# Kernel tuning notes

Measured on AMD Instinct MI355X. Metric: run time of the kernel, lower is better.

Reference implementation:

```python
import jax, jax.numpy as jnp
import numpy as np

B, P, K = 32, 1024, 20  # clouds, points per cloud, kNN neighbors
EPS = 1e-5


def knn_idx(x, k):
    # x: [B,P,d] -> indices of k nearest neighbors (squared L2, includes self), [B,P,k]
    d2 = jnp.sum(x * x, axis=-1)
    dist = d2[:, :, None] + d2[:, None, :] - 2.0 * jnp.einsum('bpd,bqd->bpq', x, x)
    _, idx = jax.lax.top_k(-dist, k)
    return idx


def edge_conv(x, idx, msg_fn):
    # gather neighbor features, build [x_i, x_j - x_i] edge features, max-aggregate
    xj = jax.vmap(lambda xb, ib: xb[ib])(x, idx)            # [B,P,K,d]
    xi = jnp.broadcast_to(x[:, :, None, :], xj.shape)       # [B,P,K,d]
    e = jnp.concatenate([xi, xj - xi], axis=-1)             # [B,P,K,2d]
    return jnp.max(msg_fn(e), axis=2)                       # [B,P,out]


def setup_inputs() -> dict:
    key = jax.random.key(0)
    ks = jax.random.split(key, 5)
    s = 0.05
    return {
        'pos': jax.random.normal(ks[0], (B * P, 3), jnp.float32),
        'W1a': jax.random.normal(ks[1], (6, 64), jnp.float32) * s,
        'b1a': jnp.zeros((64,), jnp.float32),
        'g1': jnp.ones((64,), jnp.float32),
        'be1': jnp.zeros((64,), jnp.float32),
        'W1b': jax.random.normal(ks[2], (64, 64), jnp.float32) * s,
        'b1b': jnp.zeros((64,), jnp.float32),
        'W2': jax.random.normal(ks[3], (128, 128), jnp.float32) * s,
        'b2': jnp.zeros((128,), jnp.float32),
        'Wl': jax.random.normal(ks[4], (192, 128), jnp.float32) * s,
        'bl': jnp.zeros((128,), jnp.float32),
        'batch': jnp.repeat(jnp.arange(B, dtype=jnp.int32), P),
    }


def reference(pos, W1a, b1a, g1, be1, W1b, b1b, W2, b2, Wl, bl, batch):
    # batch is uniform-sized and sorted -> fixed reshape to [B,P,.]
    x0 = pos.reshape(B, P, 3)

    def mlp1(e):  # Linear(6,64) -> BatchNorm -> ReLU -> Linear(64,64)
        h = e @ W1a + b1a
        mu = jnp.mean(h, axis=(0, 1, 2))
        var = jnp.var(h, axis=(0, 1, 2))
        h = (h - mu) * jax.lax.rsqrt(var + EPS) * g1 + be1
        h = jax.nn.relu(h)
        return h @ W1b + b1b

    x1 = edge_conv(x0, knn_idx(x0, K), mlp1)                         # [B,P,64]
    x2 = edge_conv(x1, knn_idx(x1, K), lambda e: e @ W2 + b2)        # [B,P,128]
    h = jnp.concatenate([x1, x2], axis=-1) @ Wl + bl                 # [B,P,128]
    return jnp.max(h, axis=1)                                        # global_max_pool -> [B,128]
```

## Files before the change

kernel.cpp:

```cpp
#include <hip/hip_runtime.h>
#include <cfloat>
#include <cstdint>

#define NB 32
#define NP 1024
#define NK 20
#define NPTS 32768

typedef __attribute__((ext_vector_type(8))) short bf16x8;
typedef __attribute__((ext_vector_type(4))) float f32x4;

__device__ __forceinline__ unsigned bf16rne(float v) {
  const unsigned u = __float_as_uint(v);
  return (u + 0x7fffu + ((u >> 16) & 1u)) >> 16;
}

__device__ __forceinline__ float unsort_f(unsigned s) {
  const unsigned m = (~(unsigned)((int)s >> 31)) | 0x80000000u;
  return __uint_as_float(s ^ m);
}

__global__ __launch_bounds__(256) void kd2(const float* __restrict__ x, int dim,
                                           float* __restrict__ d2) {
  int p = blockIdx.x * 256 + threadIdx.x;
  if (p >= NPTS) return;
  if (dim == 64) {
    const float4* xr = (const float4*)(x + (size_t)p * 64);
    float s = 0.f;
#pragma unroll
    for (int dq = 0; dq < 16; dq++) {
      float4 v = xr[dq];
      s = fmaf(v.x, v.x, s);
      s = fmaf(v.y, v.y, s);
      s = fmaf(v.z, v.z, s);
      s = fmaf(v.w, v.w, s);
    }
    d2[p] = s;
  } else {
    float s = 0.f;
#pragma unroll
    for (int d = 0; d < 3; d++) {
      float v = x[p * 3 + d];
      s = fmaf(v, v, s);
    }
    d2[p] = s;
  }
}

__global__ __launch_bounds__(256) void kxprep(const float* __restrict__ x,
                                              unsigned short* __restrict__ Xh,
                                              unsigned short* __restrict__ Xl) {
  const int t = blockIdx.x * 256 + threadIdx.x;
  const int p = t >> 3, g = t & 7;
  const float4* xr = (const float4*)(x + (size_t)p * 64 + g * 8);
  const float4 v0 = xr[0];
  const float4 v1 = xr[1];
  const float vv[8] = {v0.x, v0.y, v0.z, v0.w, v1.x, v1.y, v1.z, v1.w};
  unsigned short h[8], l[8];
#pragma unroll
  for (int j = 0; j < 8; j++) {
    const float z = vv[j];
    const unsigned u = __float_as_uint(z);
    const unsigned hb = (u + 0x7fffu + ((u >> 16) & 1u)) & 0xffff0000u;
    h[j] = (unsigned short)(hb >> 16);
    l[j] = (unsigned short)bf16rne(z - __uint_as_float(hb));
  }
  const int off = (((p >> 4) * 2 + (g >> 2)) * 64 + ((g & 3) << 4) + (p & 15)) * 8;
  *(uint4*)&Xh[off] = *(const uint4*)&h[0];
  *(uint4*)&Xl[off] = *(const uint4*)&l[0];
}

__device__ __forceinline__ void select20(const float* dv, unsigned long long* w,
                                         int lane, int pg, int gbase,
                                         int* __restrict__ idxo) {
  unsigned k32[16];
#pragma unroll
  for (int ii = 0; ii < 16; ii++) {
    unsigned u = __float_as_uint(dv[ii]);
    u ^= (((int)u >> 31) | 0x80000000u);
    k32[ii] = u;
  }
  unsigned lmn = k32[0];
#pragma unroll
  for (int ii = 1; ii < 16; ii++) lmn = k32[ii] < lmn ? k32[ii] : lmn;
  unsigned mn = lmn, mlm = lmn;
#pragma unroll
  for (int s = 1; s < 64; s <<= 1) {
    const unsigned a = __shfl_xor(mn, s, 64);
    const unsigned b = __shfl_xor(mlm, s, 64);
    mn = a < mn ? a : mn;
    mlm = b > mlm ? b : mlm;
  }
  unsigned lo32 = mn;
  unsigned long long hi32 = (unsigned long long)mlm + 1;
  float flo = unsort_f(mn), fhi = unsort_f(mlm);
  float clo = 0.f, chi = 140.f;
  unsigned m32 = 0;
  bool found = false;
  for (int it = 0; it < 40; ++it) {
    if (hi32 - (unsigned long long)lo32 <= 1) break;
    unsigned m;
    if (it < 6) {
      float fr = (42.f - clo) / (chi - clo);
      fr = fr < 0.04f ? 0.04f : (fr > 0.96f ? 0.96f : fr);
      const float pf = fmaf(fhi - flo, fr, flo);
      unsigned u = __float_as_uint(pf);
      u ^= (((int)u >> 31) | 0x80000000u);
      m = u;
      if (m <= lo32) m = lo32 + 1;
      if ((unsigned long long)m >= hi32) m = (unsigned)(hi32 - 1);
    } else {
      m = (unsigned)(lo32 + ((hi32 - lo32) >> 1));
    }
    int cnt = 0;
#pragma unroll
    for (int ii = 0; ii < 16; ii++) cnt += __popcll(__ballot(k32[ii] < m));
    if (cnt < 20) {
      lo32 = m;
      flo = unsort_f(m);
      clo = (float)cnt;
    } else if (cnt > 64) {
      hi32 = m;
      fhi = unsort_f(m);
      chi = (float)cnt;
    } else {
      m32 = m;
      found = true;
      break;
    }
  }

  if (found) {
    unsigned mask = 0;
#pragma unroll
    for (int ii = 0; ii < 16; ii++) mask |= (k32[ii] < m32) ? (1u << ii) : 0u;
    const int lc = __popc(mask);
    int x = lc;
#pragma unroll
    for (int s = 1; s < 64; s <<= 1) {
      const int y = __shfl_up(x, s, 64);
      if (lane >= s) x += y;
    }
    int off = x - lc;
    w[lane] = ~0ULL;
    __builtin_amdgcn_wave_barrier();
#pragma unroll
    for (int i = 0; i < 4; i++)
#pragma unroll
      for (int j = 0; j < 4; j++) {
        const int ii = i * 4 + j;
        if ((mask & (1u << ii)) && off < 64) {
          w[off] = ((unsigned long long)k32[ii] << 10) |
                   (unsigned)(i * 256 + (lane << 2) + j);
          off++;
        }
      }
    __builtin_amdgcn_wave_barrier();
    const unsigned long long K = w[lane];
    int rank = 0;
#pragma unroll
    for (int m = 0; m < 64; m++) rank += (K > w[m]) ? 1 : 0;
    if (K != ~0ULL && rank < NK)
      idxo[(size_t)pg * NK + rank] = gbase + (int)(K & 1023u);
  } else {
    unsigned long long lo64 = ((unsigned long long)lo32) << 10;
    unsigned long long hi64 = hi32 << 10;
    unsigned long long cut = hi64;
    for (int it = 0; it < 48 && (hi64 - lo64) > 1; ++it) {
      const unsigned long long m = lo64 + ((hi64 - lo64) >> 1);
      int cnt = 0;
#pragma unroll
      for (int ii = 0; ii < 16; ii++) {
        const unsigned long long key =
            ((unsigned long long)k32[ii] << 10) |
            (unsigned)(((ii >> 2) << 8) + (lane << 2) + (ii & 3));
        cnt += __popcll(__ballot(key < m));
      }
      if (cnt == 20) {
        cut = m;
        break;
      }
      if (cnt < 20)
        lo64 = m;
      else
        hi64 = m;
      cut = hi64;
    }
    int base = 0;
#pragma unroll
    for (int ii = 0; ii < 16; ii++) {
      const unsigned long long key =
          ((unsigned long long)k32[ii] << 10) |
          (unsigned)(((ii >> 2) << 8) + (lane << 2) + (ii & 3));
      const unsigned long long b = __ballot(key < cut);
      if (key < cut) {
        const int slot = base + __builtin_amdgcn_mbcnt_hi(
                                    (unsigned)(b >> 32),
                                    __builtin_amdgcn_mbcnt_lo((unsigned)b, 0));
        idxo[(size_t)pg * NK + slot] = gbase + (int)(key & 1023u);
      }
      base += __popcll(b);
    }
  }
}

__global__ __launch_bounds__(512) void kfsel1(const float* __restrict__ pos,
                                              const float* __restrict__ d2,
                                              int* __restrict__ idxo) {
  __shared__ float px[1024], py[1024], pz[1024], pd2[1024];
  __shared__ unsigned long long lw[8][64];
  const int tid = threadIdx.x;
  const int lane = tid & 63;
  const int w = tid >> 6;
  const int cloud = blockIdx.x >> 7;
  const int mb = blockIdx.x & 127;
  const int cb = cloud << 10;

  if (tid < 256) {
    const float4* ppos = (const float4*)(pos + (size_t)cb * 3 + tid * 12);
    const float4 a = ppos[0], b = ppos[1], c = ppos[2];
    *(float4*)&px[tid * 4] = make_float4(a.x, a.w, b.z, c.y);
    *(float4*)&py[tid * 4] = make_float4(a.y, b.x, b.w, c.z);
    *(float4*)&pz[tid * 4] = make_float4(a.z, b.y, c.x, c.w);
  }
  *(float2*)&pd2[tid * 2] = *(const float2*)(d2 + cb + tid * 2);
  __syncthreads();

  const int pl = mb * 8 + w;
  const float xi0 = px[pl], xi1 = py[pl], xi2 = pz[pl];
  const float dp = pd2[pl];
  float dv[16];
#pragma unroll
  for (int i = 0; i < 4; i++) {
    const float4 X = *(const float4*)&px[i * 256 + lane * 4];
    const float4 Y = *(const float4*)&py[i * 256 + lane * 4];
    const float4 Z = *(const float4*)&pz[i * 256 + lane * 4];
    const float4 Q = *(const float4*)&pd2[i * 256 + lane * 4];
    const float xs[4] = {X.x, X.y, X.z, X.w};
    const float ys[4] = {Y.x, Y.y, Y.z, Y.w};
    const float zs[4] = {Z.x, Z.y, Z.z, Z.w};
    const float qs[4] = {Q.x, Q.y, Q.z, Q.w};
#pragma unroll
    for (int j = 0; j < 4; j++) {
      float acc = 0.f;
      acc = fmaf(xi0, xs[j], acc);
      acc = fmaf(xi1, ys[j], acc);
      acc = fmaf(xi2, zs[j], acc);
      dv[i * 4 + j] = fmaf(-2.f, acc, dp + qs[j]);
    }
  }
  select20(dv, lw[w], lane, cb + pl, cb, idxo);
}

__global__ __launch_bounds__(512) void kdsel2(const unsigned short* __restrict__ Xh,
                                              const unsigned short* __restrict__ Xl,
                                              const float* __restrict__ d2,
                                              int* __restrict__ idxo) {
  __shared__ __align__(16) float Dl[16][1024];
  __shared__ unsigned long long lw[8][64];
  const int lane = threadIdx.x & 63;
  const int w = threadIdx.x >> 6;
  const int cloud = blockIdx.x & 31;
  const int rb = blockIdx.x >> 5;
  const int cb = cloud * 1024;
  const int rowb = rb * 16;

  bf16x8 Ah[2], Al[2];
#pragma unroll
  for (int ks = 0; ks < 2; ks++) {
    const int tg = (cb + rowb) >> 4;
    const size_t base = ((size_t)(tg * 2 + ks) * 64 + lane) * 8;
    Ah[ks] = *(const bf16x8*)&Xh[base];
    Al[ks] = *(const bf16x8*)&Xl[base];
  }
  float d2r[4];
#pragma unroll
  for (int r = 0; r < 4; r++) d2r[r] = d2[cb + rowb + (lane >> 4) * 4 + r];

#pragma unroll 2
  for (int nt = 0; nt < 8; nt++) {
    const int c0 = w * 128 + nt * 16;
    const int cg = cb + c0;
    bf16x8 Bh2[2], Bl2[2];
#pragma unroll
    for (int ks = 0; ks < 2; ks++) {
      const int tg = cg >> 4;
      const size_t base = ((size_t)(tg * 2 + ks) * 64 + lane) * 8;
      Bh2[ks] = *(const bf16x8*)&Xh[base];
      Bl2[ks] = *(const bf16x8*)&Xl[base];
    }
    const float d2c = d2[cg + (lane & 15)];
    f32x4 C = {0.f, 0.f, 0.f, 0.f};
    C = __builtin_amdgcn_mfma_f32_16x16x32_bf16(Ah[0], Bh2[0], C, 0, 0, 0);
    C = __builtin_amdgcn_mfma_f32_16x16x32_bf16(Ah[0], Bl2[0], C, 0, 0, 0);
    C = __builtin_amdgcn_mfma_f32_16x16x32_bf16(Al[0], Bh2[0], C, 0, 0, 0);
    C = __builtin_amdgcn_mfma_f32_16x16x32_bf16(Ah[1], Bh2[1], C, 0, 0, 0);
    C = __builtin_amdgcn_mfma_f32_16x16x32_bf16(Ah[1], Bl2[1], C, 0, 0, 0);
    C = __builtin_amdgcn_mfma_f32_16x16x32_bf16(Al[1], Bh2[1], C, 0, 0, 0);
#pragma unroll
    for (int r = 0; r < 4; r++) {
      const int row = (lane >> 4) * 4 + r;
      const int col = c0 + (lane & 15);
      Dl[row][col ^ ((row & 7) << 2)] = fmaf(-2.f, C[r], d2r[r] + d2c);
    }
  }
  __syncthreads();

  for (int pp = 0; pp < 2; pp++) {
    const int pl = w * 2 + pp;
    const int s = (pl & 7) << 2;
    float dv[16];
#pragma unroll
    for (int i = 0; i < 4; i++) {
      const float4 d4 = *(const float4*)&Dl[pl][(i * 256 + lane * 4) ^ s];
      dv[i * 4 + 0] = d4.x;
      dv[i * 4 + 1] = d4.y;
      dv[i * 4 + 2] = d4.z;
      dv[i * 4 + 3] = d4.w;
    }
    select20(dv, lw[w], lane, cb + rowb + pl, cb, idxo);
  }
}

__global__ __launch_bounds__(256) void kstats(const float* __restrict__ pos,
                                              const int* __restrict__ idx,
                                              double* __restrict__ Spart) {
  __shared__ float red[4][42];
  const int tid = threadIdx.x;
  const int w = tid >> 6;
  int p = blockIdx.x * 256 + tid;
  float xi0 = pos[p * 3], xi1 = pos[p * 3 + 1], xi2 = pos[p * 3 + 2];
  float s1[6];
  float s2[36];
#pragma unroll
  for (int a = 0; a < 6; a++) s1[a] = 0.f;
#pragma unroll
  for (int a = 0; a < 36; a++) s2[a] = 0.f;
  for (int k = 0; k < NK; k++) {
    int j = idx[p * NK + k];
    float e[6];
    e[0] = xi0;
    e[1] = xi1;
    e[2] = xi2;
    e[3] = pos[j * 3] - xi0;
    e[4] = pos[j * 3 + 1] - xi1;
    e[5] = pos[j * 3 + 2] - xi2;
#pragma unroll
    for (int a = 0; a < 6; a++) {
      s1[a] += e[a];
#pragma unroll
      for (int b = 0; b < 6; b++) s2[a * 6 + b] = fmaf(e[a], e[b], s2[a * 6 + b]);
    }
  }
#pragma unroll
  for (int a = 0; a < 6; a++) {
#pragma unroll
    for (int m = 1; m < 64; m <<= 1) s1[a] += __shfl_xor(s1[a], m, 64);
  }
#pragma unroll
  for (int a = 0; a < 36; a++) {
#pragma unroll
    for (int m = 1; m < 64; m <<= 1) s2[a] += __shfl_xor(s2[a], m, 64);
  }
  if ((tid & 63) == 0) {
#pragma unroll
    for (int a = 0; a < 6; a++) red[w][a] = s1[a];
#pragma unroll
    for (int a = 0; a < 36; a++) red[w][6 + a] = s2[a];
  }
  __syncthreads();
  if (tid < 42) {
    double t = (double)red[0][tid] + (double)red[1][tid] + (double)red[2][tid] +
               (double)red[3][tid];
    Spart[(size_t)blockIdx.x * 42 + tid] = t;
  }
}

__global__ void kbn(const double* __restrict__ Spart, const float* __restrict__ W1a,
                    const float* __restrict__ b1a, const float* __restrict__ g1,
                    const float* __restrict__ be1, const float* __restrict__ W1b,
                    float* __restrict__ ss, unsigned short* __restrict__ Bh,
                    unsigned short* __restrict__ Bl) {
  __shared__ double S[42];
  const int c = threadIdx.x;
  if (c < 42) {
    double t = 0.0;
    for (int b = 0; b < 128; b++) t += Spart[(size_t)b * 42 + c];
    S[c] = t;
  }
  for (int t = c; t < 4096; t += 256) {
    const int j = t & 7, L = (t >> 3) & 63, f = t >> 9;
    const int nt = f >> 1, ks = f & 1;
    const int k = ks * 32 + (L >> 4) * 8 + j;
    const int n = nt * 16 + (L & 15);
    const float wv = W1b[k * 64 + n];
    const unsigned u = __float_as_uint(wv);
    const unsigned hb = (u + 0x7fffu + ((u >> 16) & 1u)) & 0xffff0000u;
    Bh[t] = (unsigned short)(hb >> 16);
    Bl[t] = (unsigned short)bf16rne(wv - __uint_as_float(hb));
  }
  __syncthreads();
  if (c < 64) {
    double w[6];
#pragma unroll
    for (int d = 0; d < 6; d++) w[d] = (double)W1a[d * 64 + c];
    double b = (double)b1a[c];
    const double invN = 1.0 / (double)((size_t)NPTS * NK);
    double m1 = 0.0;
#pragma unroll
    for (int d = 0; d < 6; d++) m1 += w[d] * S[d];
    m1 *= invN;
    double q = 0.0;
#pragma unroll
    for (int a = 0; a < 6; a++)
#pragma unroll
      for (int d = 0; d < 6; d++) q += w[a] * w[d] * S[6 + a * 6 + d];
    q *= invN;
    double mu = m1 + b;
    double eh2 = q + 2.0 * b * m1 + b * b;
    double var = eh2 - mu * mu;
    if (var < 0.0) var = 0.0;
    double inv = 1.0 / sqrt(var + 1e-5);
    double sc = (double)g1[c] * inv;
    ss[c] = (float)sc;
    ss[64 + c] = (float)((double)be1[c] - mu * sc);
  }
}

#define EC1P 8
__global__ __launch_bounds__(256) void kec1(const float* __restrict__ pos,
                                            const int* __restrict__ idx,
                                            const float* __restrict__ ss,
                                            const float* __restrict__ W1a,
                                            const float* __restrict__ b1a,
                                            const unsigned short* __restrict__ Bh,
                                            const unsigned short* __restrict__ Bl,
                                            const float* __restrict__ b1b,
                                            float* __restrict__ x1) {
  __shared__ __align__(16) unsigned short Ah[4][3072];
  __shared__ __align__(16) unsigned short Al[4][3072];
  __shared__ float nbr[4][160];
  const int tid = threadIdx.x;
  const int lane = tid & 63;
  const int w = tid >> 6;
  const int p0 = blockIdx.x * EC1P + w * 2;

  unsigned short* ah = Ah[w];
  unsigned short* al = Al[w];
  float* nb = nbr[w];

  if (lane < 40) {
    const int j = idx[(size_t)p0 * NK + lane];
    nb[lane * 4 + 0] = pos[j * 3 + 0];
    nb[lane * 4 + 1] = pos[j * 3 + 1];
    nb[lane * 4 + 2] = pos[j * 3 + 2];
  }

  float wdf[3], wbt[3];
#pragma unroll
  for (int d = 0; d < 3; d++) {
    const float top = W1a[d * 64 + lane];
    const float bot = W1a[(3 + d) * 64 + lane];
    wdf[d] = top - bot;
    wbt[d] = bot;
  }
  const float b1 = b1a[lane];
  const float sc = ss[lane];
  const float sh = ss[64 + lane];
  const int lanehi = (((lane & 31) >> 3) * 128) + ((lane >> 5) * 512);
  const int lanelo = lane & 7;
  const int g3w = ((lane & 31) >> 3) + ((lane >> 5) << 2);
  __builtin_amdgcn_wave_barrier();

#pragma unroll
  for (int pp = 0; pp < 2; pp++) {
    const int p = p0 + pp;
    const float xi0 = pos[p * 3], xi1 = pos[p * 3 + 1], xi2 = pos[p * 3 + 2];
    const float pu = fmaf(xi2, wdf[2], fmaf(xi1, wdf[1], fmaf(xi0, wdf[0], b1)));
    for (int k = 0; k < NK; k++) {
      const int row = pp * NK + k;
      const float4 nbv = *(const float4*)&nb[row * 4];
      const float pv = fmaf(nbv.z, wbt[2], fmaf(nbv.y, wbt[1], nbv.x * wbt[0]));
      const float z = fmaxf(fmaf(pu + pv, sc, sh), 0.f);
      const unsigned u = __float_as_uint(z);
      const unsigned hb = (u + 0x7fffu + ((u >> 16) & 1u)) & 0xffff0000u;
      const int off =
          (row >> 4) * 1024 + lanehi + (((row & 15) ^ g3w) << 3) + lanelo;
      ah[off] = (unsigned short)(hb >> 16);
      al[off] = (unsigned short)bf16rne(z - __uint_as_float(hb));
    }
  }
  __builtin_amdgcn_wave_barrier();

  bf16x8 bh[4][2], bl[4][2];
#pragma unroll
  for (int nt = 0; nt < 4; nt++)
#pragma unroll
    for (int ks = 0; ks < 2; ks++) {
      const int base = ((nt * 2 + ks) * 64 + lane) * 8;
      bh[nt][ks] = *(const bf16x8*)&Bh[base];
      bl[nt][ks] = *(const bf16x8*)&Bl[base];
    }

  float pA[4], pB[4];
#pragma unroll
  for (int nt = 0; nt < 4; nt++) {
    pA[nt] = -FLT_MAX;
    pB[nt] = -FLT_MAX;
  }
  const int q4 = (lane >> 4) * 4;
  const int rb0 = (lane >> 4) * 128 + (((lane & 15) ^ (lane >> 4)) << 3);
  const int rb1 =
      512 + (lane >> 4) * 128 + (((lane & 15) ^ (4 + (lane >> 4))) << 3);

#pragma unroll
  for (int mt = 0; mt < 3; mt++) {
    const bf16x8 a_h0 = *(const bf16x8*)&ah[mt * 1024 + rb0];
    const bf16x8 a_l0 = *(const bf16x8*)&al[mt * 1024 + rb0];
    const bf16x8 a_h1 = *(const bf16x8*)&ah[mt * 1024 + rb1];
    const bf16x8 a_l1 = *(const bf16x8*)&al[mt * 1024 + rb1];
#pragma unroll
    for (int nt = 0; nt < 4; nt++) {
      f32x4 C = {0.f, 0.f, 0.f, 0.f};
      C = __builtin_amdgcn_mfma_f32_16x16x32_bf16(a_h0, bh[nt][0], C, 0, 0, 0);
      C = __builtin_amdgcn_mfma_f32_16x16x32_bf16(a_h0, bl[nt][0], C, 0, 0, 0);
      C = __builtin_amdgcn_mfma_f32_16x16x32_bf16(a_l0, bh[nt][0], C, 0, 0, 0);
      C = __builtin_amdgcn_mfma_f32_16x16x32_bf16(a_h1, bh[nt][1], C, 0, 0, 0);
      C = __builtin_amdgcn_mfma_f32_16x16x32_bf16(a_h1, bl[nt][1], C, 0, 0, 0);
      C = __builtin_amdgcn_mfma_f32_16x16x32_bf16(a_l1, bh[nt][1], C, 0, 0, 0);
#pragma unroll
      for (int r = 0; r < 4; r++) {
        const int row = mt * 16 + q4 + r;
        const float vv = C[r];
        if (row < NK) pA[nt] = fmaxf(pA[nt], vv);
        if (row >= NK && row < 2 * NK) pB[nt] = fmaxf(pB[nt], vv);
      }
    }
  }
#pragma unroll
  for (int s = 16; s < 64; s <<= 1) {
#pragma unroll
    for (int nt = 0; nt < 4; nt++) {
      pA[nt] = fmaxf(pA[nt], __shfl_xor(pA[nt], s, 64));
      pB[nt] = fmaxf(pB[nt], __shfl_xor(pB[nt], s, 64));
    }
  }
  if (lane < 16) {
#pragma unroll
    for (int nt = 0; nt < 4; nt++) {
      const float bb = b1b[nt * 16 + lane];
      x1[(size_t)p0 * 64 + nt * 16 + lane] = pA[nt] + bb;
      x1[(size_t)(p0 + 1) * 64 + nt * 16 + lane] = pB[nt] + bb;
    }
  }
}

__global__ __launch_bounds__(256) void kv(const float* __restrict__ x1,
                                          const float* __restrict__ W2,
                                          float* __restrict__ v) {
  const int c = threadIdx.x & 127;
  const int sub = threadIdx.x >> 7;
  float wv[64];
#pragma unroll
  for (int d = 0; d < 64; d++) wv[d] = W2[(64 + d) * 128 + c];
  const int pbase = blockIdx.x * 64 + sub * 32;
  for (int i = 0; i < 32; i++) {
    const int p = pbase + i;
    const float4* xr = (const float4*)(x1 + (size_t)p * 64);
    float a0 = 0.f, a1 = 0.f;
#pragma unroll
    for (int dq = 0; dq < 16; dq++) {
      float4 xv = xr[dq];
      a0 = fmaf(xv.x, wv[dq * 4 + 0], a0);
      a1 = fmaf(xv.y, wv[dq * 4 + 1], a1);
      a0 = fmaf(xv.z, wv[dq * 4 + 2], a0);
      a1 = fmaf(xv.w, wv[dq * 4 + 3], a1);
    }
    v[(size_t)p * 128 + c] = a0 + a1;
  }
}

__global__ __launch_bounds__(256) void kprep(const float* __restrict__ W2,
                                             const float* __restrict__ Wl,
                                             const float* __restrict__ b2,
                                             const float* __restrict__ bl,
                                             float* __restrict__ Bc,
                                             float* __restrict__ cb) {
  const int t = blockIdx.x * 256 + threadIdx.x;
  const int d = t >> 7, c = t & 127;
  float s = Wl[d * 128 + c];
  for (int e = 0; e < 128; e++)
    s = fmaf(W2[d * 128 + e] - W2[(64 + d) * 128 + e], Wl[(64 + e) * 128 + c], s);
  Bc[d * 128 + c] = s;
  Bc[(64 + 2 * d) * 128 + c] = Wl[(64 + 2 * d) * 128 + c];
  Bc[(64 + 2 * d + 1) * 128 + c] = Wl[(64 + 2 * d + 1) * 128 + c];
  if (d == 0) {
    float sb = bl[c];
    for (int e = 0; e < 128; e++) sb = fmaf(b2[e], Wl[(64 + e) * 128 + c], sb);
    cb[c] = sb;
  }
}

__global__ __launch_bounds__(256) void kprep2(const float* __restrict__ Bc,
                                              unsigned short* __restrict__ Bch,
                                              unsigned short* __restrict__ Bcl) {
  const int t = blockIdx.x * 256 + threadIdx.x;
  const int j = t & 7, L = (t >> 3) & 63, f = t >> 9;
  const int nt = f / 6, kc = f % 6;
  const int k = kc * 32 + ((L >> 4) << 3) + j;
  const int n = nt * 16 + (L & 15);
  const float wv = Bc[k * 128 + n];
  const unsigned u = __float_as_uint(wv);
  const unsigned hb = (u + 0x7fffu + ((u >> 16) & 1u)) & 0xffff0000u;
  Bch[t] = (unsigned short)(hb >> 16);
  Bcl[t] = (unsigned short)bf16rne(wv - __uint_as_float(hb));
}

__global__ __launch_bounds__(256) void kgemm(const float* __restrict__ x1,
                                             const float* __restrict__ v,
                                             const int* __restrict__ idx,
                                             const unsigned short* __restrict__ Bch,
                                             const unsigned short* __restrict__ Bcl,
                                             float* __restrict__ partial) {
  __shared__ int idxs[4][320];
  __shared__ __align__(16) float vlds[4][16][132];
  __shared__ float red[4][8][16];
  const int tid = threadIdx.x;
  const int lane = tid & 63;
  const int w = tid >> 6;
  const int cloud = blockIdx.x & 31;
  const int mb = blockIdx.x >> 5;
  const int pbase = cloud * 1024 + mb * 64;
  const int mrow = lane & 15, gsel = lane >> 4;
  const int m = w * 16 + mrow;

#pragma unroll
  for (int r = 0; r < 5; r++)
    idxs[w][r * 64 + lane] = idx[(size_t)(pbase + w * 16) * NK + r * 64 + lane];
  __builtin_amdgcn_wave_barrier();

  for (int pt = 0; pt < 16; pt++) {
    const int* ip = &idxs[w][pt * NK];
    float m0 = -FLT_MAX, m1 = -FLT_MAX;
#pragma unroll
    for (int k = 0; k < NK; k++) {
      const float2 val = *(const float2*)(v + (size_t)ip[k] * 128 + lane * 2);
      m0 = fmaxf(m0, val.x);
      m1 = fmaxf(m1, val.y);
    }
    *(float2*)&vlds[w][pt][lane * 2] = make_float2(m0, m1);
  }
  __builtin_amdgcn_wave_barrier();

  bf16x8 aH[6], aL[6];
#pragma unroll
  for (int kc = 0; kc < 2; kc++) {
    const float4* xr =
        (const float4*)(x1 + (size_t)(pbase + m) * 64 + kc * 32 + gsel * 8);
    const float4 v0 = xr[0], v1 = xr[1];
    const float vv[8] = {v0.x, v0.y, v0.z, v0.w, v1.x, v1.y, v1.z, v1.w};
    bf16x8 h, l;
#pragma unroll
    for (int j = 0; j < 8; j++) {
      const unsigned u = __float_as_uint(vv[j]);
      const unsigned hb = (u + 0x7fffu + ((u >> 16) & 1u)) & 0xffff0000u;
      h[j] = (short)(hb >> 16);
      l[j] = (short)bf16rne(vv[j] - __uint_as_float(hb));
    }
    aH[kc] = h;
    aL[kc] = l;
  }

#pragma unroll
  for (int g = 0; g < 4; g++) {
    const float* src = &vlds[w][mrow][g * 32 + gsel * 8];
    const float4 a = *(const float4*)(src);
    const float4 b = *(const float4*)(src + 4);
    const float vv[8] = {a.x, a.y, a.z, a.w, b.x, b.y, b.z, b.w};
    bf16x8 h, l;
#pragma unroll
    for (int j = 0; j < 8; j++) {
      const unsigned u = __float_as_uint(vv[j]);
      const unsigned hb = (u + 0x7fffu + ((u >> 16) & 1u)) & 0xffff0000u;
      h[j] = (short)(hb >> 16);
      l[j] = (short)bf16rne(vv[j] - __uint_as_float(hb));
    }
    aH[2 + g] = h;
    aL[2 + g] = l;
  }

  f32x4 acc[8];
#pragma unroll
  for (int nt = 0; nt < 8; nt++) acc[nt] = {0.f, 0.f, 0.f, 0.f};
#pragma unroll
  for (int nt = 0; nt < 8; nt++) {
#pragma unroll
    for (int kc = 0; kc < 6; kc++) {
      const size_t bo = ((size_t)(nt * 6 + kc) * 64 + lane) * 8;
      const bf16x8 b_h = *(const bf16x8*)&Bch[bo];
      const bf16x8 b_l = *(const bf16x8*)&Bcl[bo];
      acc[nt] = __builtin_amdgcn_mfma_f32_16x16x32_bf16(aH[kc], b_h, acc[nt], 0, 0, 0);
      acc[nt] = __builtin_amdgcn_mfma_f32_16x16x32_bf16(aH[kc], b_l, acc[nt], 0, 0, 0);
      acc[nt] = __builtin_amdgcn_mfma_f32_16x16x32_bf16(aL[kc], b_h, acc[nt], 0, 0, 0);
    }
  }

#pragma unroll
  for (int nt = 0; nt < 8; nt++) {
    float rm = fmaxf(fmaxf(acc[nt][0], acc[nt][1]), fmaxf(acc[nt][2], acc[nt][3]));
    rm = fmaxf(rm, __shfl_xor(rm, 16, 64));
    rm = fmaxf(rm, __shfl_xor(rm, 32, 64));
    if (lane < 16) red[w][nt][lane] = rm;
  }
  __syncthreads();
  if (tid < 128) {
    const int nt = tid >> 4, cc = tid & 15;
    const float m4 = fmaxf(fmaxf(red[0][nt][cc], red[1][nt][cc]),
                           fmaxf(red[2][nt][cc], red[3][nt][cc]));
    partial[(size_t)(cloud * 16 + mb) * 128 + tid] = m4;
  }
}

__global__ __launch_bounds__(256) void kred(const float* __restrict__ partial,
                                            const float* __restrict__ cb,
                                            float* __restrict__ out) {
  int t = blockIdx.x * 256 + threadIdx.x;
  int b = t >> 7, c = t & 127;
  float m = -FLT_MAX;
#pragma unroll
  for (int mb = 0; mb < 16; mb++) m = fmaxf(m, partial[(size_t)(b * 16 + mb) * 128 + c]);
  out[t] = m + cb[c];
}

extern "C" void kernel_launch(void* const* d_in, const int* in_sizes, int n_in,
                              void* d_out, int out_size, void* d_ws, size_t ws_size,
                              hipStream_t stream) {
  const float* pos = (const float*)d_in[0];
  const float* W1a = (const float*)d_in[1];
  const float* b1a = (const float*)d_in[2];
  const float* g1 = (const float*)d_in[3];
  const float* be1 = (const float*)d_in[4];
  const float* W1b = (const float*)d_in[5];
  const float* b1b = (const float*)d_in[6];
  const float* W2 = (const float*)d_in[7];
  const float* b2 = (const float*)d_in[8];
  const float* Wl = (const float*)d_in[9];
  const float* bl = (const float*)d_in[10];
  float* out = (float*)d_out;

  float* ws = (float*)d_ws;
  float* x1 = ws;
  float* v = ws + 2097152;
  int* idx = (int*)(ws + 6291456);
  float* d2b = ws + 6946816;
  double* Spart = (double*)(ws + 6979584);
  float* Bc = ws + 6990336;
  float* cb = ws + 7014912;
  float* ss = ws + 7015040;
  unsigned short* Bh = (unsigned short*)(ws + 7015168);
  unsigned short* Bl = (unsigned short*)(ws + 7017216);
  float* partial = ws + 7019264;
  unsigned short* Xfh = (unsigned short*)(ws + 7084800);
  unsigned short* Xfl = (unsigned short*)(ws + 8133376);
  unsigned short* Bch2 = (unsigned short*)(ws + 9181952);
  unsigned short* Bcl2 = (unsigned short*)(ws + 9194240);
  const size_t base = 9206528;

  if (ws_size < base * sizeof(float)) return;

  kd2<<<128, 256, 0, stream>>>(pos, 3, d2b);
  kfsel1<<<NB * 128, 512, 0, stream>>>(pos, d2b, idx);

  kstats<<<128, 256, 0, stream>>>(pos, idx, Spart);
  kbn<<<1, 256, 0, stream>>>(Spart, W1a, b1a, g1, be1, W1b, ss, Bh, Bl);
  kec1<<<NPTS / EC1P, 256, 0, stream>>>(pos, idx, ss, W1a, b1a, Bh, Bl, b1b, x1);

  kd2<<<128, 256, 0, stream>>>(x1, 64, d2b);
  kxprep<<<1024, 256, 0, stream>>>(x1, Xfh, Xfl);
  kdsel2<<<NB * 64, 512, 0, stream>>>(Xfh, Xfl, d2b, idx);

  kv<<<512, 256, 0, stream>>>(x1, W2, v);
  kprep<<<32, 256, 0, stream>>>(W2, Wl, b2, bl, Bc, cb);
  kprep2<<<96, 256, 0, stream>>>(Bc, Bch2, Bcl2);
  kgemm<<<512, 256, 0, stream>>>(x1, v, idx, Bch2, Bcl2, partial);
  kred<<<16, 256, 0, stream>>>(partial, cb, out);
}
```

Measured before the change: 302.5 us.

## Halve kdsel2 LDS distance tile by processing columns in two register-held halves

```diff
diff --git a/kernel.cpp b/kernel.cpp
--- a/kernel.cpp
+++ b/kernel.cpp
@@ -70,16 +70,9 @@
   *(uint4*)&Xl[off] = *(const uint4*)&l[0];
 }
 
-__device__ __forceinline__ void select20(const float* dv, unsigned long long* w,
-                                         int lane, int pg, int gbase,
-                                         int* __restrict__ idxo) {
-  unsigned k32[16];
-#pragma unroll
-  for (int ii = 0; ii < 16; ii++) {
-    unsigned u = __float_as_uint(dv[ii]);
-    u ^= (((int)u >> 31) | 0x80000000u);
-    k32[ii] = u;
-  }
+__device__ __forceinline__ void select20k(const unsigned* k32, unsigned long long* w,
+                                          int lane, int pg, int gbase,
+                                          int* __restrict__ idxo) {
   unsigned lmn = k32[0];
 #pragma unroll
   for (int ii = 1; ii < 16; ii++) lmn = k32[ii] < lmn ? k32[ii] : lmn;
@@ -204,6 +197,19 @@
   }
 }
 
+__device__ __forceinline__ void select20(const float* dv, unsigned long long* w,
+                                         int lane, int pg, int gbase,
+                                         int* __restrict__ idxo) {
+  unsigned k32[16];
+#pragma unroll
+  for (int ii = 0; ii < 16; ii++) {
+    unsigned u = __float_as_uint(dv[ii]);
+    u ^= (((int)u >> 31) | 0x80000000u);
+    k32[ii] = u;
+  }
+  select20k(k32, w, lane, pg, gbase, idxo);
+}
+
 __global__ __launch_bounds__(512) void kfsel1(const float* __restrict__ pos,
                                               const float* __restrict__ d2,
                                               int* __restrict__ idxo) {
@@ -252,11 +258,11 @@
   select20(dv, lw[w], lane, cb + pl, cb, idxo);
 }
 
-__global__ __launch_bounds__(512) void kdsel2(const unsigned short* __restrict__ Xh,
-                                              const unsigned short* __restrict__ Xl,
-                                              const float* __restrict__ d2,
-                                              int* __restrict__ idxo) {
-  __shared__ __align__(16) float Dl[16][1024];
+__global__ __launch_bounds__(512, 8) void kdsel2(const unsigned short* __restrict__ Xh,
+                                                 const unsigned short* __restrict__ Xl,
+                                                 const float* __restrict__ d2,
+                                                 int* __restrict__ idxo) {
+  __shared__ __align__(16) float Dl[16][512];
   __shared__ unsigned long long lw[8][64];
   const int lane = threadIdx.x & 63;
   const int w = threadIdx.x >> 6;
@@ -277,48 +283,76 @@
 #pragma unroll
   for (int r = 0; r < 4; r++) d2r[r] = d2[cb + rowb + (lane >> 4) * 4 + r];
 
-#pragma unroll 2
-  for (int nt = 0; nt < 8; nt++) {
-    const int c0 = w * 128 + nt * 16;
-    const int cg = cb + c0;
-    bf16x8 Bh2[2], Bl2[2];
-#pragma unroll
-    for (int ks = 0; ks < 2; ks++) {
-      const int tg = cg >> 4;
-      const size_t base = ((size_t)(tg * 2 + ks) * 64 + lane) * 8;
-      Bh2[ks] = *(const bf16x8*)&Xh[base];
-      Bl2[ks] = *(const bf16x8*)&Xl[base];
-    }
-    const float d2c = d2[cg + (lane & 15)];
-    f32x4 C = {0.f, 0.f, 0.f, 0.f};
-    C = __builtin_amdgcn_mfma_f32_16x16x32_bf16(Ah[0], Bh2[0], C, 0, 0, 0);
-    C = __builtin_amdgcn_mfma_f32_16x16x32_bf16(Ah[0], Bl2[0], C, 0, 0, 0);
-    C = __builtin_amdgcn_mfma_f32_16x16x32_bf16(Al[0], Bh2[0], C, 0, 0, 0);
-    C = __builtin_amdgcn_mfma_f32_16x16x32_bf16(Ah[1], Bh2[1], C, 0, 0, 0);
-    C = __builtin_amdgcn_mfma_f32_16x16x32_bf16(Ah[1], Bl2[1], C, 0, 0, 0);
-    C = __builtin_amdgcn_mfma_f32_16x16x32_bf16(Al[1], Bh2[1], C, 0, 0, 0);
-#pragma unroll
-    for (int r = 0; r < 4; r++) {
-      const int row = (lane >> 4) * 4 + r;
-      const int col = c0 + (lane & 15);
-      Dl[row][col ^ ((row & 7) << 2)] = fmaf(-2.f, C[r], d2r[r] + d2c);
-    }
-  }
-  __syncthreads();
+  unsigned kk0[2][8];
+
+  for (int h = 0; h < 2; h++) {
+#pragma unroll
+    for (int nt = 0; nt < 4; nt++) {
+      const int c0 = w * 64 + nt * 16;
+      const int cg = cb + h * 512 + c0;
+      bf16x8 Bh2[2], Bl2[2];
+#pragma unroll
+      for (int ks = 0; ks < 2; ks++) {
+        const int tg = cg >> 4;
+        const size_t base = ((size_t)(tg * 2 + ks) * 64 + lane) * 8;
+        Bh2[ks] = *(const bf16x8*)&Xh[base];
+        Bl2[ks] = *(const bf16x8*)&Xl[base];
+      }
+      const float d2c = d2[cg + (lane & 15)];
+      f32x4 C = {0.f, 0.f, 0.f, 0.f};
+      C = __builtin_amdgcn_mfma_f32_16x16x32_bf16(Ah[0], Bh2[0], C, 0, 0, 0);
+      C = __builtin_amdgcn_mfma_f32_16x16x32_bf16(Ah[0], Bl2[0], C, 0, 0, 0);
+      C = __builtin_amdgcn_mfma_f32_16x16x32_bf16(Al[0], Bh2[0], C, 0, 0, 0);
+      C = __builtin_amdgcn_mfma_f32_16x16x32_bf16(Ah[1], Bh2[1], C, 0, 0, 0);
+      C = __builtin_amdgcn_mfma_f32_16x16x32_bf16(Ah[1], Bl2[1], C, 0, 0, 0);
+      C = __builtin_amdgcn_mfma_f32_16x16x32_bf16(Al[1], Bh2[1], C, 0, 0, 0);
+#pragma unroll
+      for (int r = 0; r < 4; r++) {
+        const int row = (lane >> 4) * 4 + r;
+        const int col = c0 + (lane & 15);
+        Dl[row][col ^ ((row & 7) << 2)] = fmaf(-2.f, C[r], d2r[r] + d2c);
+      }
+    }
+    __syncthreads();
+    if (h == 0) {
+#pragma unroll
+      for (int pp = 0; pp < 2; pp++) {
+        const int pl = w * 2 + pp;
+        const int s = (pl & 7) << 2;
+#pragma unroll
+        for (int i2 = 0; i2 < 2; i2++) {
+          const float4 d4 = *(const float4*)&Dl[pl][(i2 * 256 + lane * 4) ^ s];
+          const float dvv[4] = {d4.x, d4.y, d4.z, d4.w};
+#pragma unroll
+          for (int j = 0; j < 4; j++) {
+            unsigned u = __float_as_uint(dvv[j]);
+            u ^= (((int)u >> 31) | 0x80000000u);
+            kk0[pp][i2 * 4 + j] = u;
+          }
+        }
+      }
+      __syncthreads();
+    }
+  }
 
   for (int pp = 0; pp < 2; pp++) {
     const int pl = w * 2 + pp;
     const int s = (pl & 7) << 2;
-    float dv[16];
-#pragma unroll
-    for (int i = 0; i < 4; i++) {
-      const float4 d4 = *(const float4*)&Dl[pl][(i * 256 + lane * 4) ^ s];
-      dv[i * 4 + 0] = d4.x;
-      dv[i * 4 + 1] = d4.y;
-      dv[i * 4 + 2] = d4.z;
-      dv[i * 4 + 3] = d4.w;
-    }
-    select20(dv, lw[w], lane, cb + rowb + pl, cb, idxo);
+    unsigned k32[16];
+#pragma unroll
+    for (int ii = 0; ii < 8; ii++) k32[ii] = kk0[pp][ii];
+#pragma unroll
+    for (int i2 = 0; i2 < 2; i2++) {
+      const float4 d4 = *(const float4*)&Dl[pl][(i2 * 256 + lane * 4) ^ s];
+      const float dvv[4] = {d4.x, d4.y, d4.z, d4.w};
+#pragma unroll
+      for (int j = 0; j < 4; j++) {
+        unsigned u = __float_as_uint(dvv[j]);
+        u ^= (((int)u >> 31) | 0x80000000u);
+        k32[8 + i2 * 4 + j] = u;
+      }
+    }
+    select20k(k32, lw[w], lane, cb + rowb + pl, cb, idxo);
   }
 }
 
```

After: 343.1 us. +13.4%, slower.
